# Kernel tuning notes

Measured on AMD Instinct MI355X. Metric: run time of the kernel, lower is better.

Reference implementation:

```python
import jax, jax.numpy as jnp
import numpy as np

EPS = 1e-5
# NOTE: TransmorpherLayer2d passes (dim_head, num_heads) into TiedAxialSelfAttention2d(num_heads, dim_head),
# so with init dim_head=64, num_heads=8 the attention effectively uses H=64 heads of C=8 channels each.
H = 64
C = 8


def _ln_ch(x, w, b):
    # AxialLayerNorm over channel dim (dim=1) of [B, D, S, L]
    m = x.mean(axis=1, keepdims=True)
    v = x.var(axis=1, keepdims=True)
    return (x - m) * jax.lax.rsqrt(v + EPS) * w[None, :, None, None] + b[None, :, None, None]


def _conv1x1(x, W, b):
    # Conv2d kernel_size=1: pointwise channel mix. W: [out, in], x: [B, in, S, L]
    return jnp.einsum('od,bdsl->bosl', W, x) + b[None, :, None, None]


def setup_inputs() -> dict:
    key = jax.random.key(0)
    ks = jax.random.split(key, 8)
    B, D, S, L, F = 1, 512, 64, 256, 2048
    g = lambda k, shape: jax.random.normal(k, shape, jnp.float32) * 0.02
    return {
        'x': jax.random.normal(ks[0], (B, D, S, L), jnp.float32),
        'w_row': g(ks[1], (3 * D, D)), 'b_row': jnp.zeros((3 * D,), jnp.float32),
        'w_col': g(ks[2], (3 * D, D)), 'b_col': jnp.zeros((3 * D,), jnp.float32),
        'w_an1': jnp.ones((D,), jnp.float32), 'b_an1': jnp.zeros((D,), jnp.float32),
        'w_an2': jnp.ones((D,), jnp.float32), 'b_an2': jnp.zeros((D,), jnp.float32),
        'w_ff1': g(ks[3], (F, D)), 'b_ff1': jnp.zeros((F,), jnp.float32),
        'w_ff2': g(ks[4], (D, F)), 'b_ff2': jnp.zeros((D,), jnp.float32),
        'w_ln1': jnp.ones((D,), jnp.float32), 'b_ln1': jnp.zeros((D,), jnp.float32),
        'w_ln2': jnp.ones((D,), jnp.float32), 'b_ln2': jnp.zeros((D,), jnp.float32),
    }


def _forward(x, w_row, b_row, w_col, b_col, w_an1, b_an1, w_an2, b_an2,
             w_ff1, b_ff1, w_ff2, b_ff2, w_ln1, b_ln1, w_ln2, b_ln2):
    B, D, S, L = x.shape
    # ---- tied row attention (attention tied across the S axis; no 1/sqrt scaling in source) ----
    qkv = _conv1x1(x, w_row, b_row)
    q, k, v = [t.reshape(B, H, C, S, L) for t in jnp.split(qkv, 3, axis=1)]
    row_attn = jax.nn.softmax(jnp.einsum('bhcsi,bhcsj->bhij', q, k), axis=-1)  # [B,H,L,L]
    row_out = jnp.einsum('bhij,bhdsj->bhdsi', row_attn, v).reshape(B, D, S, L)
    out = _ln_ch(x + row_out, w_an1, b_an1)
    # ---- column attention (softmax over key index j = dim -2) ----
    qkv = _conv1x1(out, w_col, b_col)
    q, k, v = [t.reshape(B, H, C, S, L) for t in jnp.split(qkv, 3, axis=1)]
    col_attn = jax.nn.softmax(jnp.einsum('bhcil,bhcjl->bhijl', q, k), axis=-2)  # [B,H,S,S,L]
    col_out = jnp.einsum('bhijl,bhdjl->bhdil', col_attn, v).reshape(B, D, S, L)
    attn_out = _ln_ch(out + col_out, w_an2, b_an2)
    # ---- layer body. Source bug kept faithfully: the attention residual `x + dropout1(out)`
    # is computed then discarded; norm1 is applied to the attention output only. ----
    h = _ln_ch(attn_out, w_ln1, b_ln1)
    ff = _conv1x1(jax.nn.relu(_conv1x1(h, w_ff1, b_ff1)), w_ff2, b_ff2)
    return _ln_ch(h + ff, w_ln2, b_ln2)


def reference(x, w_row, b_row, w_col, b_col, w_an1, b_an1, w_an2, b_an2,
              w_ff1, b_ff1, w_ff2, b_ff2, w_ln1, b_ln1, w_ln2, b_ln2):
    return _forward(x, w_row, b_row, w_col, b_col, w_an1, b_an1, w_an2, b_an2,
                    w_ff1, b_ff1, w_ff2, b_ff2, w_ln1, b_ln1, w_ln2, b_ln2)
```

## Files before the change

kernel.cpp:

```cpp
#include <hip/hip_runtime.h>
#include <hip/hip_bf16.h>

using s16x8 = __attribute__((ext_vector_type(8))) short;
using f32x4 = __attribute__((ext_vector_type(4))) float;
using u32x2 = __attribute__((ext_vector_type(2))) unsigned;

__device__ __forceinline__ ushort f2bf(float f) {
  union { float f; unsigned u; } v; v.f = f;
  unsigned r = v.u + 0x7fffu + ((v.u >> 16) & 1u);
  return (ushort)(r >> 16);
}
__device__ __forceinline__ float bf2f(ushort u) {
  return __uint_as_float(((unsigned)u) << 16);
}
__device__ __forceinline__ void gload16(const void* g, void* l) {
  __builtin_amdgcn_global_load_lds(
      (const __attribute__((address_space(1))) void*)g,
      (__attribute__((address_space(3))) void*)l, 16, 0, 0);
}

template<int AF, int BF, bool BIAS, bool RELU, int OUT, bool TRC>
__global__ __launch_bounds__(256, 3)
void gemm(void* __restrict__ Cv, const ushort* __restrict__ A,
          const ushort* __restrict__ B, const float* __restrict__ bias,
          int K, int lda, int ldb, int ldc, long sA, long sB, long sC)
{
  __shared__ ushort As[2][5120];
  __shared__ ushort Bs[2][5120];
  const int tid  = threadIdx.x;
  const int lane = tid & 63, wid = tid >> 6;
  const int gx = gridDim.x, gy = gridDim.y;
  const int lin = blockIdx.y * gx + blockIdx.x;
  int mb, nb;
  if ((gx & 7) == 0) {
    const int xcd = lin & 7, idx = lin >> 3, gxp = gx >> 3;
    nb = xcd * gxp + idx / gy;
    mb = idx % gy;
  } else {
    const int nwg = gx * gy;
    const int swz = ((nwg & 7) == 0) ? ((lin & 7) * (nwg >> 3) + (lin >> 3)) : lin;
    mb = swz / gx; nb = swz % gx;
  }
  const int m0 = mb * 128, n0 = nb * 128;
  A += (long)blockIdx.z * sA;
  B += (long)blockIdx.z * sB;

  const int wm = (wid >> 1) * 64, wn = (wid & 1) * 64;
  const int fr = lane & 15, kg = lane >> 4;

  f32x4 acc[4][4];
#pragma unroll
  for (int i = 0; i < 4; ++i)
#pragma unroll
    for (int j = 0; j < 4; ++j)
#pragma unroll
      for (int r = 0; r < 4; ++r) acc[i][j][r] = 0.f;

  auto stageT = [&](const ushort* __restrict__ G, int ld, int c0,
                    ushort* lds, int k0) {
#pragma unroll
    for (int c = 0; c < 2; ++c) {
      const int nb2 = wid * 2 + c;
      const ushort* gp = G + (long)(k0 + (lane >> 1)) * ld + c0 + nb2 * 16 + (lane & 1) * 8;
      gload16(gp, lds + nb2 * 512);
    }
  };
  auto loadN = [&](const ushort* __restrict__ G, int ld, int r0, int k0,
                   uint4& x, uint4& y) {
    const ushort* gp = G + (long)(r0 + (tid >> 1)) * ld + k0 + (tid & 1) * 8;
    x = *(const uint4*)gp;
    y = *(const uint4*)(gp + 16);
  };
  auto writeN = [&](ushort* lds, uint4 x, uint4 y) {
    ushort* p = lds + (tid >> 1) * 40 + (tid & 1) * 8;
    *(uint4*)p = x;
    *(uint4*)(p + 16) = y;
  };
  auto fragN = [&](const ushort* lds, int row) {
    union { s16x8 f; u32x2 h[2]; } u;
    const ushort* p = lds + row * 40 + kg * 4;
    u.h[0] = *(const u32x2*)p;
    u.h[1] = *(const u32x2*)(p + 16);
    return u.f;
  };
  auto fragT = [&](const ushort* lds, int rb) {
    union { s16x8 f; u32x2 h[2]; } u;
    unsigned base = (unsigned)(unsigned long long)(lds + rb * 512) + lane * 8;
    asm volatile("ds_read_b64_tr_b16 %0, %1" : "=v"(u.h[0]) : "v"(base));
    asm volatile("ds_read_b64_tr_b16 %0, %1 offset:512" : "=v"(u.h[1]) : "v"(base));
    return u.f;
  };

  const int NT = K >> 5;
  uint4 ax, ay, bx, by;

  if constexpr (AF == 0) { loadN(A, lda, m0, 0, ax, ay); writeN(As[0], ax, ay); }
  else                   { stageT(A, lda, m0, As[0], 0); }
  if constexpr (BF == 0) { loadN(B, ldb, n0, 0, bx, by); writeN(Bs[0], bx, by); }
  else                   { stageT(B, ldb, n0, Bs[0], 0); }
  __syncthreads();

  for (int t = 0; t < NT; ++t) {
    const int cur = t & 1, nxt = cur ^ 1;
    const bool pre = (t + 1) < NT;
    if (pre) {
      if constexpr (AF == 0) loadN(A, lda, m0, (t + 1) << 5, ax, ay);
      else                   stageT(A, lda, m0, As[nxt], (t + 1) << 5);
      if constexpr (BF == 0) loadN(B, ldb, n0, (t + 1) << 5, bx, by);
      else                   stageT(B, ldb, n0, Bs[nxt], (t + 1) << 5);
    }
    s16x8 af[4], bv[4];
#pragma unroll
    for (int m = 0; m < 4; ++m) {
      if constexpr (AF == 0) af[m] = fragN(As[cur], wm + m * 16 + fr);
      else                   af[m] = fragT(As[cur], (wm >> 4) + m);
    }
#pragma unroll
    for (int n = 0; n < 4; ++n) {
      if constexpr (BF == 0) bv[n] = fragN(Bs[cur], wn + n * 16 + fr);
      else                   bv[n] = fragT(Bs[cur], (wn >> 4) + n);
    }
    if constexpr (AF == 1 || BF == 1) {
      asm volatile("s_waitcnt lgkmcnt(0)");
      __builtin_amdgcn_sched_barrier(0);
    }
    __builtin_amdgcn_s_setprio(1);
#pragma unroll
    for (int m = 0; m < 4; ++m)
#pragma unroll
      for (int n = 0; n < 4; ++n)
        acc[m][n] = __builtin_amdgcn_mfma_f32_16x16x32_bf16(af[m], bv[n], acc[m][n], 0, 0, 0);
    __builtin_amdgcn_s_setprio(0);
    if (pre) {
      if constexpr (AF == 0) writeN(As[nxt], ax, ay);
      if constexpr (BF == 0) writeN(Bs[nxt], bx, by);
    }
    __syncthreads();
  }

#pragma unroll
  for (int m = 0; m < 4; ++m) {
    const int rowb = m0 + wm + m * 16 + kg * 4;
#pragma unroll
    for (int n = 0; n < 4; ++n) {
      const int col = n0 + wn + n * 16 + fr;
      f32x4 v = acc[m][n];
      if constexpr (BIAS) {
#pragma unroll
        for (int r = 0; r < 4; ++r) v[r] += bias[rowb + r];
      }
      if constexpr (RELU) {
#pragma unroll
        for (int r = 0; r < 4; ++r) v[r] = fmaxf(v[r], 0.f);
      }
      if constexpr (TRC) {
        if constexpr (OUT == 0) {
          float* C = (float*)Cv + (long)blockIdx.z * sC;
          float4 s; s.x = v[0]; s.y = v[1]; s.z = v[2]; s.w = v[3];
          *(float4*)(C + (long)col * ldc + rowb) = s;
        } else {
          ushort* C = (ushort*)Cv + (long)blockIdx.z * sC;
          ushort4 s; s.x = f2bf(v[0]); s.y = f2bf(v[1]); s.z = f2bf(v[2]); s.w = f2bf(v[3]);
          *(ushort4*)(C + (long)col * ldc + rowb) = s;
        }
      } else if constexpr (OUT == 0) {
        float* C = (float*)Cv + (long)blockIdx.z * sC;
#pragma unroll
        for (int r = 0; r < 4; ++r) C[(long)(rowb + r) * ldc + col] = v[r];
      } else {
        ushort* C = (ushort*)Cv + (long)blockIdx.z * sC;
#pragma unroll
        for (int r = 0; r < 4; ++r) C[(long)(rowb + r) * ldc + col] = f2bf(v[r]);
      }
    }
  }
}

__global__ __launch_bounds__(256)
void cvt_kernel(const float4* __restrict__ in, ushort4* __restrict__ out, int n4) {
  int i = blockIdx.x * 256 + threadIdx.x;
  if (i < n4) {
    float4 f = in[i];
    ushort4 u; u.x = f2bf(f.x); u.y = f2bf(f.y); u.z = f2bf(f.z); u.w = f2bf(f.w);
    out[i] = u;
  }
}

__global__ __launch_bounds__(256)
void softmax_kernel(const float* __restrict__ S, ushort* __restrict__ P) {
  const int row = blockIdx.x * 4 + (threadIdx.x >> 6);
  const int lane = threadIdx.x & 63;
  float4 v = *(const float4*)(S + (long)row * 256 + lane * 4);
  float mx = fmaxf(fmaxf(v.x, v.y), fmaxf(v.z, v.w));
#pragma unroll
  for (int off = 32; off; off >>= 1) mx = fmaxf(mx, __shfl_xor(mx, off));
  v.x = __expf(v.x - mx); v.y = __expf(v.y - mx);
  v.z = __expf(v.z - mx); v.w = __expf(v.w - mx);
  float s = v.x + v.y + v.z + v.w;
#pragma unroll
  for (int off = 32; off; off >>= 1) s += __shfl_xor(s, off);
  const float r = 1.f / s;
  ushort4 o;
  o.x = f2bf(v.x * r); o.y = f2bf(v.y * r); o.z = f2bf(v.z * r); o.w = f2bf(v.w * r);
  *(ushort4*)(P + (long)row * 256 + lane * 4) = o;
}

__global__ __launch_bounds__(256)
void colattn_kernel(const ushort* __restrict__ qkv, ushort* __restrict__ out) {
  __shared__ float q[4][8][64], kk[4][8][64], vv[4][8][64];
  const int lin = blockIdx.x;
  const int swz = (lin & 7) * 512 + (lin >> 3);
  const int h = swz >> 6;
  const int l0 = (swz & 63) * 4;
  const int tid = threadIdx.x;
  for (int i = tid; i < 1536; i += 256) {
    int m = i >> 9;
    int e = i & 511;
    int c = e >> 6, s = e & 63;
    ushort4 u = *(const ushort4*)(qkv + (long)(m * 512 + h * 8 + c) * 16384 + s * 256 + l0);
    float* dst = (m == 0) ? &q[0][0][0] : (m == 1) ? &kk[0][0][0] : &vv[0][0][0];
    dst[e] = bf2f(u.x); dst[512 + e] = bf2f(u.y);
    dst[1024 + e] = bf2f(u.z); dst[1536 + e] = bf2f(u.w);
  }
  __syncthreads();
  const int li = tid >> 6, lane = tid & 63;
  float qi[8];
#pragma unroll
  for (int c = 0; c < 8; ++c) qi[c] = q[li][c][lane];
  float sc[64];
#pragma unroll
  for (int j4 = 0; j4 < 16; ++j4) {
    float ax = 0.f, ay = 0.f, az = 0.f, aw = 0.f;
#pragma unroll
    for (int c = 0; c < 8; ++c) {
      float4 k4 = *(const float4*)&kk[li][c][j4 * 4];
      ax = fmaf(qi[c], k4.x, ax); ay = fmaf(qi[c], k4.y, ay);
      az = fmaf(qi[c], k4.z, az); aw = fmaf(qi[c], k4.w, aw);
    }
    sc[j4 * 4 + 0] = ax; sc[j4 * 4 + 1] = ay;
    sc[j4 * 4 + 2] = az; sc[j4 * 4 + 3] = aw;
  }
  float mx = sc[0];
#pragma unroll
  for (int j = 1; j < 64; ++j) mx = fmaxf(mx, sc[j]);
  float sum = 0.f;
#pragma unroll
  for (int j = 0; j < 64; ++j) { sc[j] = __expf(sc[j] - mx); sum += sc[j]; }
  const float rs = 1.f / sum;
  float o[8];
#pragma unroll
  for (int c = 0; c < 8; ++c) o[c] = 0.f;
#pragma unroll
  for (int j4 = 0; j4 < 16; ++j4) {
    const float px = sc[j4 * 4 + 0], py = sc[j4 * 4 + 1];
    const float pz = sc[j4 * 4 + 2], pw = sc[j4 * 4 + 3];
#pragma unroll
    for (int c = 0; c < 8; ++c) {
      float4 v4 = *(const float4*)&vv[li][c][j4 * 4];
      o[c] = fmaf(px, v4.x, fmaf(py, v4.y, fmaf(pz, v4.z, fmaf(pw, v4.w, o[c]))));
    }
  }
#pragma unroll
  for (int c = 0; c < 8; ++c) q[li][c][lane] = o[c] * rs;
  __syncthreads();
  for (int i = tid; i < 512; i += 256) {
    int c = i >> 6, s = i & 63;
    ushort4 u;
    u.x = f2bf(q[0][c][s]); u.y = f2bf(q[1][c][s]);
    u.z = f2bf(q[2][c][s]); u.w = f2bf(q[3][c][s]);
    *(ushort4*)(out + (long)(h * 8 + c) * 16384 + s * 256 + l0) = u;
  }
}

template<bool RES, int OM>
__global__ __launch_bounds__(1024)
void ln_kernel(void* __restrict__ outv, const ushort* __restrict__ a,
               const ushort* __restrict__ b, const float* __restrict__ w,
               const float* __restrict__ bias) {
  __shared__ float red[2][16][64];
  const int lane = threadIdx.x & 63, seg = threadIdx.x >> 6;
  const long n = (long)blockIdx.x * 64 + lane;
  const int d0 = seg * 32;
  float v[32];
  float s1 = 0.f, s2 = 0.f;
#pragma unroll
  for (int i = 0; i < 32; ++i) {
    float t = bf2f(a[(long)(d0 + i) * 16384 + n]);
    if constexpr (RES) t += bf2f(b[(long)(d0 + i) * 16384 + n]);
    v[i] = t; s1 += t; s2 += t * t;
  }
  red[0][seg][lane] = s1; red[1][seg][lane] = s2;
  __syncthreads();
  s1 = 0.f; s2 = 0.f;
#pragma unroll
  for (int s = 0; s < 16; ++s) { s1 += red[0][s][lane]; s2 += red[1][s][lane]; }
  const float mean = s1 * (1.f / 512.f);
  const float var = s2 * (1.f / 512.f) - mean * mean;
  const float rstd = rsqrtf(var + 1e-5f);
#pragma unroll
  for (int i = 0; i < 32; ++i) {
    float o = (v[i] - mean) * rstd * w[d0 + i] + bias[d0 + i];
    if constexpr (OM == 0) ((ushort*)outv)[(long)(d0 + i) * 16384 + n] = f2bf(o);
    else                   ((float*)outv)[(long)(d0 + i) * 16384 + n] = o;
  }
}

__global__ __launch_bounds__(1024)
void ln_fuse_kernel(ushort* __restrict__ out, const ushort* __restrict__ a,
                    const ushort* __restrict__ b,
                    const float* __restrict__ w1, const float* __restrict__ b1,
                    const float* __restrict__ w2, const float* __restrict__ b2) {
  __shared__ float red[2][16][64];
  const int lane = threadIdx.x & 63, seg = threadIdx.x >> 6;
  const long n = (long)blockIdx.x * 64 + lane;
  const int d0 = seg * 32;
  float v[32];
  float s1 = 0.f, s2 = 0.f;
#pragma unroll
  for (int i = 0; i < 32; ++i) {
    float t = bf2f(a[(long)(d0 + i) * 16384 + n]) + bf2f(b[(long)(d0 + i) * 16384 + n]);
    v[i] = t; s1 += t; s2 += t * t;
  }
  red[0][seg][lane] = s1; red[1][seg][lane] = s2;
  __syncthreads();
  s1 = 0.f; s2 = 0.f;
#pragma unroll
  for (int s = 0; s < 16; ++s) { s1 += red[0][s][lane]; s2 += red[1][s][lane]; }
  float mean = s1 * (1.f / 512.f);
  float var = s2 * (1.f / 512.f) - mean * mean;
  float rstd = rsqrtf(var + 1e-5f);
  __syncthreads();
  s1 = 0.f; s2 = 0.f;
#pragma unroll
  for (int i = 0; i < 32; ++i) {
    float y = (v[i] - mean) * rstd * w1[d0 + i] + b1[d0 + i];
    v[i] = y; s1 += y; s2 += y * y;
  }
  red[0][seg][lane] = s1; red[1][seg][lane] = s2;
  __syncthreads();
  s1 = 0.f; s2 = 0.f;
#pragma unroll
  for (int s = 0; s < 16; ++s) { s1 += red[0][s][lane]; s2 += red[1][s][lane]; }
  mean = s1 * (1.f / 512.f);
  var = s2 * (1.f / 512.f) - mean * mean;
  rstd = rsqrtf(var + 1e-5f);
#pragma unroll
  for (int i = 0; i < 32; ++i) {
    float o = (v[i] - mean) * rstd * w2[d0 + i] + b2[d0 + i];
    out[(long)(d0 + i) * 16384 + n] = f2bf(o);
  }
}

extern "C" void kernel_launch(void* const* d_in, const int* in_sizes, int n_in,
                              void* d_out, int out_size, void* d_ws, size_t ws_size,
                              hipStream_t stream) {
  const float* x     = (const float*)d_in[0];
  const float* w_row = (const float*)d_in[1];
  const float* b_row = (const float*)d_in[2];
  const float* w_col = (const float*)d_in[3];
  const float* b_col = (const float*)d_in[4];
  const float* w_an1 = (const float*)d_in[5];
  const float* b_an1 = (const float*)d_in[6];
  const float* w_an2 = (const float*)d_in[7];
  const float* b_an2 = (const float*)d_in[8];
  const float* w_ff1 = (const float*)d_in[9];
  const float* b_ff1 = (const float*)d_in[10];
  const float* w_ff2 = (const float*)d_in[11];
  const float* b_ff2 = (const float*)d_in[12];
  const float* w_ln1 = (const float*)d_in[13];
  const float* b_ln1 = (const float*)d_in[14];
  const float* w_ln2 = (const float*)d_in[15];
  const float* b_ln2 = (const float*)d_in[16];
  float* outp = (float*)d_out;

  char* Wb = (char*)d_ws;
  ushort* big    = (ushort*)Wb;
  float*  sc     = (float*)(Wb + 71303168ull);
  ushort* colbf  = (ushort*)(Wb + 71303168ull);
  ushort* P      = (ushort*)(Wb + 90177536ull);
  ushort* xbf    = (ushort*)(Wb + 100663296ull);
  ushort* ff2bf  = (ushort*)(Wb + 100663296ull);
  ushort* rowbf  = (ushort*)(Wb + 118489088ull);
  ushort* out1bf = (ushort*)(Wb + 136314880ull);
  ushort* hbf    = (ushort*)(Wb + 154140672ull);
  ushort* wrowb  = (ushort*)(Wb + 171966464ull);
  ushort* wcolb = wrowb + 786432;
  ushort* wff1b = wcolb + 786432;
  ushort* wff2b = wff1b + 1048576;

  const dim3 blk(256);
  const long HQ = 131072;
  const long HS = 65536;

  cvt_kernel<<<8192, blk, 0, stream>>>((const float4*)x, (ushort4*)xbf, 2097152);
  cvt_kernel<<<768,  blk, 0, stream>>>((const float4*)w_row, (ushort4*)wrowb, 196608);
  cvt_kernel<<<768,  blk, 0, stream>>>((const float4*)w_col, (ushort4*)wcolb, 196608);
  cvt_kernel<<<1024, blk, 0, stream>>>((const float4*)w_ff1, (ushort4*)wff1b, 262144);
  cvt_kernel<<<1024, blk, 0, stream>>>((const float4*)w_ff2, (ushort4*)wff2b, 262144);

  gemm<0,1,true,false,1,false><<<dim3(128, 12, 1), blk, 0, stream>>>(
      big, wrowb, xbf, b_row, 512, 512, 16384, 16384, 0, 0, 0);
  gemm<1,1,false,false,0,false><<<dim3(2, 2, 64), blk, 0, stream>>>(
      sc, big, big + (long)512 * 16384, nullptr, 512, 256, 256, 256, HQ, HQ, HS);
  softmax_kernel<<<4096, blk, 0, stream>>>(sc, P);
  gemm<0,0,false,false,1,true><<<dim3(4, 2, 64), blk, 0, stream>>>(
      rowbf, P, big + (long)1024 * 16384, nullptr, 256, 256, 256, 256, HS, HQ, HQ);
  ln_kernel<true, 0><<<256, dim3(1024), 0, stream>>>(out1bf, xbf, rowbf, w_an1, b_an1);
  gemm<0,1,true,false,1,false><<<dim3(128, 12, 1), blk, 0, stream>>>(
      big, wcolb, out1bf, b_col, 512, 512, 16384, 16384, 0, 0, 0);
  colattn_kernel<<<4096, blk, 0, stream>>>(big, colbf);
  ln_fuse_kernel<<<256, dim3(1024), 0, stream>>>(hbf, out1bf, colbf,
                                                 w_an2, b_an2, w_ln1, b_ln1);
  gemm<0,1,true,true,1,false><<<dim3(128, 16, 1), blk, 0, stream>>>(
      big, wff1b, hbf, b_ff1, 512, 512, 16384, 16384, 0, 0, 0);
  gemm<0,1,true,false,1,false><<<dim3(128, 4, 1), blk, 0, stream>>>(
      ff2bf, wff2b, big, b_ff2, 2048, 2048, 16384, 16384, 0, 0, 0);
  ln_kernel<true, 1><<<256, dim3(1024), 0, stream>>>(outp, hbf, ff2bf, w_ln2, b_ln2);
}
```

Measured before the change: 433.7 us.

## Merge weight conversions, double-buffer LDS reads in column attention, move score buffer

Combines the four weight fp32-to-bf16 conversion launches into a single kernel that picks its source by block index, removing three launches. In the column-attention kernel, the K and V loops now load the next float4 group from LDS into registers while the current one is being used, so LDS latency overlaps with FMAs at the cost of more registers. The row-attention score buffer is moved to a different workspace offset, which changes aliasing with the qkv buffer.

```diff
diff --git a/kernel.cpp b/kernel.cpp
--- a/kernel.cpp
+++ b/kernel.cpp
@@ -187,6 +187,22 @@
 }
 
 __global__ __launch_bounds__(256)
+void cvtw_kernel(const float4* __restrict__ w0, ushort4* __restrict__ o0,
+                 const float4* __restrict__ w1, ushort4* __restrict__ o1,
+                 const float4* __restrict__ w2, ushort4* __restrict__ o2,
+                 const float4* __restrict__ w3, ushort4* __restrict__ o3) {
+  const int b = blockIdx.x;
+  const float4* in; ushort4* out; int i;
+  if (b < 768)       { in = w0; out = o0; i = b * 256 + threadIdx.x; }
+  else if (b < 1536) { in = w1; out = o1; i = (b - 768) * 256 + threadIdx.x; }
+  else if (b < 2560) { in = w2; out = o2; i = (b - 1536) * 256 + threadIdx.x; }
+  else               { in = w3; out = o3; i = (b - 2560) * 256 + threadIdx.x; }
+  float4 f = in[i];
+  ushort4 u; u.x = f2bf(f.x); u.y = f2bf(f.y); u.z = f2bf(f.z); u.w = f2bf(f.w);
+  out[i] = u;
+}
+
+__global__ __launch_bounds__(256)
 void softmax_kernel(const float* __restrict__ S, ushort* __restrict__ P) {
   const int row = blockIdx.x * 4 + (threadIdx.x >> 6);
   const int lane = threadIdx.x & 63;
@@ -228,17 +244,27 @@
 #pragma unroll
   for (int c = 0; c < 8; ++c) qi[c] = q[li][c][lane];
   float sc[64];
-#pragma unroll
-  for (int j4 = 0; j4 < 16; ++j4) {
-    float ax = 0.f, ay = 0.f, az = 0.f, aw = 0.f;
-#pragma unroll
-    for (int c = 0; c < 8; ++c) {
-      float4 k4 = *(const float4*)&kk[li][c][j4 * 4];
-      ax = fmaf(qi[c], k4.x, ax); ay = fmaf(qi[c], k4.y, ay);
-      az = fmaf(qi[c], k4.z, az); aw = fmaf(qi[c], k4.w, aw);
-    }
-    sc[j4 * 4 + 0] = ax; sc[j4 * 4 + 1] = ay;
-    sc[j4 * 4 + 2] = az; sc[j4 * 4 + 3] = aw;
+  {
+    float4 ka[8], kb[8];
+#pragma unroll
+    for (int c = 0; c < 8; ++c) ka[c] = *(const float4*)&kk[li][c][0];
+#pragma unroll
+    for (int j4 = 0; j4 < 16; ++j4) {
+      const float4* cur = (j4 & 1) ? kb : ka;
+      float4* nxt = (j4 & 1) ? ka : kb;
+      if (j4 < 15) {
+#pragma unroll
+        for (int c = 0; c < 8; ++c) nxt[c] = *(const float4*)&kk[li][c][(j4 + 1) * 4];
+      }
+      float ax = 0.f, ay = 0.f, az = 0.f, aw = 0.f;
+#pragma unroll
+      for (int c = 0; c < 8; ++c) {
+        ax = fmaf(qi[c], cur[c].x, ax); ay = fmaf(qi[c], cur[c].y, ay);
+        az = fmaf(qi[c], cur[c].z, az); aw = fmaf(qi[c], cur[c].w, aw);
+      }
+      sc[j4 * 4 + 0] = ax; sc[j4 * 4 + 1] = ay;
+      sc[j4 * 4 + 2] = az; sc[j4 * 4 + 3] = aw;
+    }
   }
   float mx = sc[0];
 #pragma unroll
@@ -250,14 +276,25 @@
   float o[8];
 #pragma unroll
   for (int c = 0; c < 8; ++c) o[c] = 0.f;
-#pragma unroll
-  for (int j4 = 0; j4 < 16; ++j4) {
-    const float px = sc[j4 * 4 + 0], py = sc[j4 * 4 + 1];
-    const float pz = sc[j4 * 4 + 2], pw = sc[j4 * 4 + 3];
-#pragma unroll
-    for (int c = 0; c < 8; ++c) {
-      float4 v4 = *(const float4*)&vv[li][c][j4 * 4];
-      o[c] = fmaf(px, v4.x, fmaf(py, v4.y, fmaf(pz, v4.z, fmaf(pw, v4.w, o[c]))));
+  {
+    float4 va[8], vb[8];
+#pragma unroll
+    for (int c = 0; c < 8; ++c) va[c] = *(const float4*)&vv[li][c][0];
+#pragma unroll
+    for (int j4 = 0; j4 < 16; ++j4) {
+      const float4* cur = (j4 & 1) ? vb : va;
+      float4* nxt = (j4 & 1) ? va : vb;
+      if (j4 < 15) {
+#pragma unroll
+        for (int c = 0; c < 8; ++c) nxt[c] = *(const float4*)&vv[li][c][(j4 + 1) * 4];
+      }
+      const float px = sc[j4 * 4 + 0], py = sc[j4 * 4 + 1];
+      const float pz = sc[j4 * 4 + 2], pw = sc[j4 * 4 + 3];
+#pragma unroll
+      for (int c = 0; c < 8; ++c) {
+        o[c] = fmaf(px, cur[c].x, fmaf(py, cur[c].y,
+               fmaf(pz, cur[c].z, fmaf(pw, cur[c].w, o[c]))));
+      }
     }
   }
 #pragma unroll
@@ -375,7 +412,7 @@
 
   char* Wb = (char*)d_ws;
   ushort* big    = (ushort*)Wb;
-  float*  sc     = (float*)(Wb + 71303168ull);
+  float*  sc     = (float*)(Wb + 50331648ull);
   ushort* colbf  = (ushort*)(Wb + 71303168ull);
   ushort* P      = (ushort*)(Wb + 90177536ull);
   ushort* xbf    = (ushort*)(Wb + 100663296ull);
@@ -393,10 +430,9 @@
   const long HS = 65536;
 
   cvt_kernel<<<8192, blk, 0, stream>>>((const float4*)x, (ushort4*)xbf, 2097152);
-  cvt_kernel<<<768,  blk, 0, stream>>>((const float4*)w_row, (ushort4*)wrowb, 196608);
-  cvt_kernel<<<768,  blk, 0, stream>>>((const float4*)w_col, (ushort4*)wcolb, 196608);
-  cvt_kernel<<<1024, blk, 0, stream>>>((const float4*)w_ff1, (ushort4*)wff1b, 262144);
-  cvt_kernel<<<1024, blk, 0, stream>>>((const float4*)w_ff2, (ushort4*)wff2b, 262144);
+  cvtw_kernel<<<3584, blk, 0, stream>>>(
+      (const float4*)w_row, (ushort4*)wrowb, (const float4*)w_col, (ushort4*)wcolb,
+      (const float4*)w_ff1, (ushort4*)wff1b, (const float4*)w_ff2, (ushort4*)wff2b);
 
   gemm<0,1,true,false,1,false><<<dim3(128, 12, 1), blk, 0, stream>>>(
       big, wrowb, xbf, b_row, 512, 512, 16384, 16384, 0, 0, 0);
```

Result: no change. 426.7 us (-1.6%).
